# Performance work log

Measured on AMD Instinct MI355X. Metric: run time of the kernel, lower is better.

Reference implementation:

```python
import jax, jax.numpy as jnp
import numpy as np

NUM_HEADS = 16


def setup_inputs() -> dict:
    key = jax.random.key(0)
    k1, k2, k3 = jax.random.split(key, 3)
    B, S, D = 4, 2048, 1024
    hidden_states = jax.random.normal(k1, (B, S, D), dtype=jnp.float32)
    w_qkv = jax.random.normal(k2, (D, 3 * D), dtype=jnp.float32) * (1.0 / np.sqrt(D))
    w_out = jax.random.normal(k3, (D, D), dtype=jnp.float32) * (1.0 / np.sqrt(D))
    return {"hidden_states": hidden_states, "w_qkv": w_qkv, "w_out": w_out}


def reference(hidden_states, w_qkv, w_out):
    B, S, D = hidden_states.shape
    H = NUM_HEADS
    d = D // H
    # fused QKV projection: [B, S, 3D] -> [3, B, S, H, d]
    qkv = (hidden_states @ w_qkv).reshape(B, S, 3, H, d)
    q, k, v = jnp.moveaxis(qkv, 2, 0)  # each [B, S, H, d]
    scale = 1.0 / np.sqrt(d).astype(np.float32)
    scores = jnp.einsum("bqhd,bkhd->bhqk", q, k) * scale  # [B, H, S, S]
    attn = jax.nn.softmax(scores, axis=-1)
    ctx = jnp.einsum("bhqk,bkhd->bqhd", attn, v).reshape(B, S, D)
    return ctx @ w_out
```

## Files before the change

kernel.cpp:

```cpp
#include <hip/hip_runtime.h>
#include <hip/hip_bf16.h>
#include <math.h>

typedef __bf16 bf16;
typedef __bf16 bf16x4 __attribute__((ext_vector_type(4)));
typedef __bf16 bf16x8 __attribute__((ext_vector_type(8)));
typedef float  f32x4  __attribute__((ext_vector_type(4)));

#define B_  4
#define S_  2048
#define D_  1024
#define H_  16
#define DH  64
#define M_  (B_*S_)
#define BH_ (B_*H_)

#define QSCALE 0.18033688011112042f

__device__ __forceinline__ void glds16(const bf16* g, bf16* l) {
  __builtin_amdgcn_global_load_lds((const __attribute__((address_space(1))) void*)g,
                                   (__attribute__((address_space(3))) void*)l, 16, 0, 0);
}

__global__ __launch_bounds__(256) void prep(const float* __restrict__ hidden, bf16* __restrict__ hb,
                                            const float* __restrict__ wqkv, const float* __restrict__ wout,
                                            bf16* __restrict__ wqkvT, bf16* __restrict__ woutT) {
  int bx = blockIdx.x, tid = threadIdx.x;
  if (bx < 8192) {
    int i = (bx * 256 + tid) * 4;
    float4 v = *(const float4*)(hidden + i);
    bf16x4 o = { (bf16)v.x, (bf16)v.y, (bf16)v.z, (bf16)v.w };
    *(bf16x4*)(hb + i) = o;
    return;
  }
  __shared__ float tile[32][33];
  int t = bx - 8192;
  const float* in; bf16* out; int C, c0, r0;
  if (t < 96 * 32) { in = wqkv; out = wqkvT; C = 3072; c0 = (t % 96) * 32; r0 = (t / 96) * 32; }
  else { t -= 96 * 32;  in = wout; out = woutT; C = 1024; c0 = (t % 32) * 32; r0 = (t / 32) * 32; }
  int tx = tid & 31, ty = tid >> 5;
  #pragma unroll
  for (int i = ty; i < 32; i += 8) tile[i][tx] = in[(size_t)(r0 + i) * C + c0 + tx];
  __syncthreads();
  #pragma unroll
  for (int i = ty; i < 32; i += 8) out[(size_t)(c0 + i) * D_ + r0 + tx] = (bf16)tile[tx][i];
}

#define LDA2 32
#define SUB  (128 * LDA2)

__device__ __forceinline__ void gemm_core(const bf16* __restrict__ A, const bf16* __restrict__ Bt,
                                          int m0, int n0, bf16* As, bf16* Bs,
                                          int tid, f32x4 acc[4][4]) {
  int wave = tid >> 6, lane = tid & 63, quad = lane >> 4, l16 = lane & 15;
  int wm = (wave >> 1) * 64, wn = (wave & 1) * 64;
  int lr = lane >> 2, lc = (lane & 3) * 8;
  const bf16* gA = A  + (size_t)(m0 + wave * 32 + lr) * D_ + lc;
  const bf16* gB = Bt + (size_t)(n0 + wave * 32 + lr) * D_ + lc;
  bf16* lA = As + wave * 32 * LDA2;
  bf16* lB = Bs + wave * 32 * LDA2;
  for (int k0 = 0; k0 < D_; k0 += 64) {
    #pragma unroll
    for (int h = 0; h < 2; h++) {
      int kk = k0 + h * 32;
      glds16(gA + kk,           lA + h * SUB);
      glds16(gA + kk + 16 * D_, lA + h * SUB + 16 * LDA2);
      glds16(gB + kk,           lB + h * SUB);
      glds16(gB + kk + 16 * D_, lB + h * SUB + 16 * LDA2);
    }
    __syncthreads();
    #pragma unroll
    for (int h = 0; h < 2; h++) {
      bf16x8 af[4], bff[4];
      #pragma unroll
      for (int i = 0; i < 4; i++) af[i]  = *(const bf16x8*)(As + h * SUB + (wm + i * 16 + l16) * LDA2 + quad * 8);
      #pragma unroll
      for (int j = 0; j < 4; j++) bff[j] = *(const bf16x8*)(Bs + h * SUB + (wn + j * 16 + l16) * LDA2 + quad * 8);
      #pragma unroll
      for (int i = 0; i < 4; i++)
        #pragma unroll
        for (int j = 0; j < 4; j++)
          acc[i][j] = __builtin_amdgcn_mfma_f32_16x16x32_bf16(af[i], bff[j], acc[i][j], 0, 0, 0);
    }
    __syncthreads();
  }
}

__global__ __launch_bounds__(256) void gemm_qkv(const bf16* __restrict__ A, const bf16* __restrict__ Bt,
                                                bf16* __restrict__ Qb, bf16* __restrict__ Kb,
                                                bf16* __restrict__ Vtb) {
  __shared__ __attribute__((aligned(16))) bf16 As[2 * SUB];
  __shared__ __attribute__((aligned(16))) bf16 Bs[2 * SUB];
  int tid = threadIdx.x;
  int m0 = blockIdx.y * 128, n0 = blockIdx.x * 128;
  f32x4 acc[4][4] = {};
  gemm_core(A, Bt, m0, n0, As, Bs, tid, acc);
  int wave = tid >> 6, lane = tid & 63, quad = lane >> 4, l16 = lane & 15;
  int wm = (wave >> 1) * 64, wn = (wave & 1) * 64;
  int which = n0 >> 10;
  if (which == 2) {
    #pragma unroll
    for (int i = 0; i < 4; i++) {
      int mb = m0 + wm + i * 16 + quad * 4;
      int b = mb >> 11, s = mb & 2047;
      #pragma unroll
      for (int j = 0; j < 4; j++) {
        int n = n0 + wn + j * 16 + l16;
        int h = (n >> 6) & 15, dd = n & 63;
        bf16x4 v4 = { (bf16)acc[i][j][0], (bf16)acc[i][j][1], (bf16)acc[i][j][2], (bf16)acc[i][j][3] };
        *(bf16x4*)(Vtb + ((size_t)(b * H_ + h) * DH + dd) * S_ + s) = v4;
      }
    }
  } else {
    bf16* dst = (which == 0) ? Qb : Kb;
    float sc = (which == 0) ? QSCALE : 1.0f;
    #pragma unroll
    for (int i = 0; i < 4; i++) {
      #pragma unroll
      for (int j = 0; j < 4; j++) {
        int n = n0 + wn + j * 16 + l16;
        int h = (n >> 6) & 15, dd = n & 63;
        #pragma unroll
        for (int r = 0; r < 4; r++) {
          int m = m0 + wm + i * 16 + quad * 4 + r;
          int b = m >> 11, s = m & 2047;
          dst[(((size_t)(b * H_ + h)) * S_ + s) * DH + dd] = (bf16)(acc[i][j][r] * sc);
        }
      }
    }
  }
}

__global__ __launch_bounds__(256) void gemm_out(const bf16* __restrict__ A, const bf16* __restrict__ Bt,
                                                float* __restrict__ C) {
  __shared__ __attribute__((aligned(16))) bf16 As[2 * SUB];
  __shared__ __attribute__((aligned(16))) bf16 Bs[2 * SUB];
  int tid = threadIdx.x;
  int m0 = blockIdx.x * 128, n0 = blockIdx.y * 128;
  f32x4 acc[4][4] = {};
  gemm_core(A, Bt, m0, n0, As, Bs, tid, acc);
  int wave = tid >> 6, lane = tid & 63, quad = lane >> 4, l16 = lane & 15;
  int wm = (wave >> 1) * 64, wn = (wave & 1) * 64;
  #pragma unroll
  for (int i = 0; i < 4; i++)
    #pragma unroll
    for (int j = 0; j < 4; j++) {
      int n = n0 + wn + j * 16 + l16;
      #pragma unroll
      for (int r = 0; r < 4; r++) {
        int m = m0 + wm + i * 16 + quad * 4 + r;
        C[(size_t)m * D_ + n] = acc[i][j][r];
      }
    }
}

#define NT  (S_ / 64)

#define KVSW(row, col) (((row) * 64) + ((col) ^ (((row) & 7) << 3)))
#define PSW(row, col)  (((row) * 32) + ((col) ^ ((((row) >> 1) & 3) << 3)))

__global__ __launch_bounds__(256, 2) void attn(const bf16* __restrict__ Qb, const bf16* __restrict__ Kb,
                                               const bf16* __restrict__ Vtb, bf16* __restrict__ ctx) {
  __shared__ __attribute__((aligned(16))) bf16 Ks[2][64 * 64];
  __shared__ __attribute__((aligned(16))) bf16 Vs[2][64 * 64];
  __shared__ __attribute__((aligned(16))) bf16 Ps[4][64 * 32];
  int tid = threadIdx.x;
  int wave = tid >> 6, lane = tid & 63, quad = lane >> 4, l16 = lane & 15;
  int bh = blockIdx.x;
  int b = bh >> 4, h = bh & 15;
  int q0 = blockIdx.y * 256 + wave * 64;
  const bf16* Qp = Qb  + (size_t)bh * S_ * DH;
  const bf16* Kp = Kb  + (size_t)bh * S_ * DH;
  const bf16* Vp = Vtb + (size_t)bh * DH * S_;

  int srow = tid >> 3, scc = (tid & 7) << 3;
  int swz = KVSW(srow, scc);

  bf16x8 qf[4][2];
  #pragma unroll
  for (int nq = 0; nq < 4; nq++)
    #pragma unroll
    for (int ks = 0; ks < 2; ks++)
      qf[nq][ks] = *(const bf16x8*)(Qp + (size_t)(q0 + nq * 16 + l16) * DH + ks * 32 + quad * 8);

  bf16 one1 = (bf16)1.0f;
  bf16x8 onesf = { one1, one1, one1, one1, one1, one1, one1, one1 };

  f32x4 o[4][4] = {};
  f32x4 oden[4] = {};

  {
    bf16x8 k0a = *(const bf16x8*)(Kp + (size_t)srow * DH + scc);
    bf16x8 k0b = *(const bf16x8*)(Kp + (size_t)(32 + srow) * DH + scc);
    bf16x8 v0a = *(const bf16x8*)(Vp + (size_t)srow * S_ + scc);
    bf16x8 v0b = *(const bf16x8*)(Vp + (size_t)(32 + srow) * S_ + scc);
    *(bf16x8*)(Ks[0] + swz)             = k0a;
    *(bf16x8*)(Ks[0] + swz + 32 * 64)   = k0b;
    *(bf16x8*)(Vs[0] + swz)             = v0a;
    *(bf16x8*)(Vs[0] + swz + 32 * 64)   = v0b;
  }

  for (int kt = 0; kt < NT; kt++) {
    int cur = kt & 1;
    __syncthreads();

    bf16x8 ka, kb2, va, vb;
    if (kt + 1 < NT) {
      const bf16* Kn = Kp + (size_t)(kt + 1) * 64 * DH;
      const bf16* Vn = Vp + (size_t)(kt + 1) * 64;
      ka  = *(const bf16x8*)(Kn + (size_t)srow * DH + scc);
      kb2 = *(const bf16x8*)(Kn + (size_t)(32 + srow) * DH + scc);
      va  = *(const bf16x8*)(Vn + (size_t)srow * S_ + scc);
      vb  = *(const bf16x8*)(Vn + (size_t)(32 + srow) * S_ + scc);
    }

    bf16x8 vf[4][2];
    #pragma unroll
    for (int td = 0; td < 4; td++)
      #pragma unroll
      for (int ks = 0; ks < 2; ks++)
        vf[td][ks] = *(const bf16x8*)(Vs[cur] + KVSW(td * 16 + l16, ks * 32 + quad * 8));

    #pragma unroll
    for (int hh = 0; hh < 2; hh++) {
      #pragma unroll
      for (int kq2 = 0; kq2 < 2; kq2++) {
        int kq = hh * 2 + kq2;
        bf16x8 kfr[2];
        #pragma unroll
        for (int ks = 0; ks < 2; ks++)
          kfr[ks] = *(const bf16x8*)(Ks[cur] + KVSW(kq * 16 + l16, ks * 32 + quad * 8));
        #pragma unroll
        for (int nq = 0; nq < 4; nq++) {
          f32x4 st = {};
          __builtin_amdgcn_s_setprio(1);
          st = __builtin_amdgcn_mfma_f32_16x16x32_bf16(kfr[0], qf[nq][0], st, 0, 0, 0);
          st = __builtin_amdgcn_mfma_f32_16x16x32_bf16(kfr[1], qf[nq][1], st, 0, 0, 0);
          __builtin_amdgcn_s_setprio(0);
          bf16x4 pk;
          #pragma unroll
          for (int r = 0; r < 4; r++) pk[r] = (bf16)__builtin_amdgcn_exp2f(st[r]);
          *(bf16x4*)(&Ps[wave][PSW(nq * 16 + l16, kq2 * 16 + quad * 4)]) = pk;
        }
      }
      #pragma unroll
      for (int nq = 0; nq < 4; nq++) {
        bf16x8 pf = *(const bf16x8*)(&Ps[wave][PSW(nq * 16 + l16, quad * 8)]);
        __builtin_amdgcn_s_setprio(1);
        oden[nq] = __builtin_amdgcn_mfma_f32_16x16x32_bf16(pf, onesf, oden[nq], 0, 0, 0);
        #pragma unroll
        for (int td = 0; td < 4; td++)
          o[nq][td] = __builtin_amdgcn_mfma_f32_16x16x32_bf16(pf, vf[td][hh], o[nq][td], 0, 0, 0);
        __builtin_amdgcn_s_setprio(0);
      }
    }

    if (kt + 1 < NT) {
      int nxt = cur ^ 1;
      *(bf16x8*)(Ks[nxt] + swz)           = ka;
      *(bf16x8*)(Ks[nxt] + swz + 32 * 64) = kb2;
      *(bf16x8*)(Vs[nxt] + swz)           = va;
      *(bf16x8*)(Vs[nxt] + swz + 32 * 64) = vb;
    }
  }

  #pragma unroll
  for (int nq = 0; nq < 4; nq++) {
    #pragma unroll
    for (int r = 0; r < 4; r++) {
      float inv = 1.0f / oden[nq][r];
      int q = q0 + nq * 16 + quad * 4 + r;
      #pragma unroll
      for (int td = 0; td < 4; td++) {
        int dd = td * 16 + l16;
        ctx[((size_t)(b * S_) + q) * D_ + h * DH + dd] = (bf16)(o[nq][td][r] * inv);
      }
    }
  }
}

extern "C" void kernel_launch(void* const* d_in, const int* in_sizes, int n_in,
                              void* d_out, int out_size, void* d_ws, size_t ws_size,
                              hipStream_t stream) {
  (void)in_sizes; (void)n_in; (void)out_size; (void)ws_size;
  const float* hidden = (const float*)d_in[0];
  const float* w_qkv  = (const float*)d_in[1];
  const float* w_out  = (const float*)d_in[2];
  float* out = (float*)d_out;

  char* ws = (char*)d_ws;
  size_t off = 0;
  bf16* hb    = (bf16*)(ws + off); off += (size_t)M_ * D_ * 2;
  bf16* wqkvT = (bf16*)(ws + off); off += (size_t)3 * D_ * D_ * 2;
  bf16* woutT = (bf16*)(ws + off); off += (size_t)D_ * D_ * 2;
  bf16* Qb    = (bf16*)(ws + off); off += (size_t)M_ * D_ * 2;
  bf16* Kb    = (bf16*)(ws + off); off += (size_t)M_ * D_ * 2;
  bf16* Vtb   = (bf16*)(ws + off); off += (size_t)M_ * D_ * 2;
  bf16* ctxb  = hb;

  prep<<<8192 + 96 * 32 + 32 * 32, 256, 0, stream>>>(hidden, hb, w_qkv, w_out, wqkvT, woutT);
  gemm_qkv<<<dim3(3 * D_ / 128, M_ / 128), 256, 0, stream>>>(hb, wqkvT, Qb, Kb, Vtb);
  attn<<<dim3(BH_, S_ / 256), 256, 0, stream>>>(Qb, Kb, Vtb, ctxb);
  gemm_out<<<dim3(M_ / 128, D_ / 128), 256, 0, stream>>>(ctxb, woutT, out);
}
```

Baseline: 258.4 us.

## Fuse hidden fp32->bf16 cast into QKV GEMM, remap blocks, vectorize epilogues

The separate pass that casts hidden states to bf16 is removed; the QKV GEMM now loads fp32 A tiles directly, converts them in registers and writes them to LDS. Block indices are remapped so that neighbouring M tiles land on the same XCD for better L2 reuse. For Q/K and the output GEMM, the MFMA operands are swapped so the epilogues can write vectorized bf16x4 or f32x4 stores instead of scalar ones. The s_setprio hints are dropped from the attention loop. The fused A path loses the async global-to-LDS copy and reads twice the bytes per A tile inside the GEMM.

```diff
diff --git a/kernel.cpp b/kernel.cpp
--- a/kernel.cpp
+++ b/kernel.cpp
@@ -22,19 +22,10 @@
                                    (__attribute__((address_space(3))) void*)l, 16, 0, 0);
 }
 
-__global__ __launch_bounds__(256) void prep(const float* __restrict__ hidden, bf16* __restrict__ hb,
-                                            const float* __restrict__ wqkv, const float* __restrict__ wout,
+__global__ __launch_bounds__(256) void prep(const float* __restrict__ wqkv, const float* __restrict__ wout,
                                             bf16* __restrict__ wqkvT, bf16* __restrict__ woutT) {
-  int bx = blockIdx.x, tid = threadIdx.x;
-  if (bx < 8192) {
-    int i = (bx * 256 + tid) * 4;
-    float4 v = *(const float4*)(hidden + i);
-    bf16x4 o = { (bf16)v.x, (bf16)v.y, (bf16)v.z, (bf16)v.w };
-    *(bf16x4*)(hb + i) = o;
-    return;
-  }
   __shared__ float tile[32][33];
-  int t = bx - 8192;
+  int t = blockIdx.x, tid = threadIdx.x;
   const float* in; bf16* out; int C, c0, r0;
   if (t < 96 * 32) { in = wqkv; out = wqkvT; C = 3072; c0 = (t % 96) * 32; r0 = (t / 96) * 32; }
   else { t -= 96 * 32;  in = wout; out = woutT; C = 1024; c0 = (t % 32) * 32; r0 = (t / 32) * 32; }
@@ -49,9 +40,10 @@
 #define LDA2 32
 #define SUB  (128 * LDA2)
 
-__device__ __forceinline__ void gemm_core(const bf16* __restrict__ A, const bf16* __restrict__ Bt,
-                                          int m0, int n0, bf16* As, bf16* Bs,
-                                          int tid, f32x4 acc[4][4]) {
+template<bool SW>
+__device__ __forceinline__ void core128(const bf16* __restrict__ A, const bf16* __restrict__ Bt,
+                                        int m0, int n0, bf16* As, bf16* Bs,
+                                        int tid, f32x4 acc[4][4]) {
   int wave = tid >> 6, lane = tid & 63, quad = lane >> 4, l16 = lane & 15;
   int wm = (wave >> 1) * 64, wn = (wave & 1) * 64;
   int lr = lane >> 2, lc = (lane & 3) * 8;
@@ -79,26 +71,86 @@
       #pragma unroll
       for (int i = 0; i < 4; i++)
         #pragma unroll
-        for (int j = 0; j < 4; j++)
-          acc[i][j] = __builtin_amdgcn_mfma_f32_16x16x32_bf16(af[i], bff[j], acc[i][j], 0, 0, 0);
-    }
-    __syncthreads();
-  }
-}
-
-__global__ __launch_bounds__(256) void gemm_qkv(const bf16* __restrict__ A, const bf16* __restrict__ Bt,
+        for (int j = 0; j < 4; j++) {
+          if constexpr (SW)
+            acc[j][i] = __builtin_amdgcn_mfma_f32_16x16x32_bf16(bff[j], af[i], acc[j][i], 0, 0, 0);
+          else
+            acc[i][j] = __builtin_amdgcn_mfma_f32_16x16x32_bf16(af[i], bff[j], acc[i][j], 0, 0, 0);
+        }
+    }
+    __syncthreads();
+  }
+}
+
+template<bool SW>
+__device__ __forceinline__ void coreA32(const float* __restrict__ Af, const bf16* __restrict__ Bt,
+                                        int m0, int n0, bf16* As, bf16* Bs,
+                                        int tid, f32x4 acc[4][4]) {
+  int wave = tid >> 6, lane = tid & 63, quad = lane >> 4, l16 = lane & 15;
+  int wm = (wave >> 1) * 64, wn = (wave & 1) * 64;
+  int lr = lane >> 2, lc = (lane & 3) * 8;
+  const float* gA = Af + (size_t)(m0 + wave * 32 + lr) * D_ + lc;
+  const bf16*  gB = Bt + (size_t)(n0 + wave * 32 + lr) * D_ + lc;
+  bf16* lB = Bs + wave * 32 * LDA2;
+  bf16* wA = As + wave * 32 * LDA2 + lane * 8;
+  for (int k0 = 0; k0 < D_; k0 += 64) {
+    #pragma unroll
+    for (int h = 0; h < 2; h++) {
+      int kk = k0 + h * 32;
+      glds16(gB + kk,           lB + h * SUB);
+      glds16(gB + kk + 16 * D_, lB + h * SUB + 16 * LDA2);
+    }
+    #pragma unroll
+    for (int h = 0; h < 2; h++) {
+      int kk = k0 + h * 32;
+      #pragma unroll
+      for (int c = 0; c < 2; c++) {
+        const float* src = gA + kk + (size_t)(c * 16) * D_;
+        float4 v0 = *(const float4*)(src);
+        float4 v1 = *(const float4*)(src + 4);
+        bf16x8 w = { (bf16)v0.x, (bf16)v0.y, (bf16)v0.z, (bf16)v0.w,
+                     (bf16)v1.x, (bf16)v1.y, (bf16)v1.z, (bf16)v1.w };
+        *(bf16x8*)(wA + h * SUB + c * 16 * LDA2) = w;
+      }
+    }
+    __syncthreads();
+    #pragma unroll
+    for (int h = 0; h < 2; h++) {
+      bf16x8 af[4], bff[4];
+      #pragma unroll
+      for (int i = 0; i < 4; i++) af[i]  = *(const bf16x8*)(As + h * SUB + (wm + i * 16 + l16) * LDA2 + quad * 8);
+      #pragma unroll
+      for (int j = 0; j < 4; j++) bff[j] = *(const bf16x8*)(Bs + h * SUB + (wn + j * 16 + l16) * LDA2 + quad * 8);
+      #pragma unroll
+      for (int i = 0; i < 4; i++)
+        #pragma unroll
+        for (int j = 0; j < 4; j++) {
+          if constexpr (SW)
+            acc[j][i] = __builtin_amdgcn_mfma_f32_16x16x32_bf16(bff[j], af[i], acc[j][i], 0, 0, 0);
+          else
+            acc[i][j] = __builtin_amdgcn_mfma_f32_16x16x32_bf16(af[i], bff[j], acc[i][j], 0, 0, 0);
+        }
+    }
+    __syncthreads();
+  }
+}
+
+__global__ __launch_bounds__(256) void gemm_qkv(const float* __restrict__ hidden, const bf16* __restrict__ Bt,
                                                 bf16* __restrict__ Qb, bf16* __restrict__ Kb,
                                                 bf16* __restrict__ Vtb) {
   __shared__ __attribute__((aligned(16))) bf16 As[2 * SUB];
   __shared__ __attribute__((aligned(16))) bf16 Bs[2 * SUB];
   int tid = threadIdx.x;
-  int m0 = blockIdx.y * 128, n0 = blockIdx.x * 128;
-  f32x4 acc[4][4] = {};
-  gemm_core(A, Bt, m0, n0, As, Bs, tid, acc);
+  int lin = blockIdx.y * 24 + blockIdx.x;
+  int xcd = lin & 7, idx = lin >> 3;
+  int m0 = ((xcd << 3) + (idx / 24)) * 128;
+  int n0 = (idx % 24) * 128;
   int wave = tid >> 6, lane = tid & 63, quad = lane >> 4, l16 = lane & 15;
   int wm = (wave >> 1) * 64, wn = (wave & 1) * 64;
   int which = n0 >> 10;
+  f32x4 acc[4][4] = {};
   if (which == 2) {
+    coreA32<false>(hidden, Bt, m0, n0, As, Bs, tid, acc);
     #pragma unroll
     for (int i = 0; i < 4; i++) {
       int mb = m0 + wm + i * 16 + quad * 4;
@@ -112,20 +164,20 @@
       }
     }
   } else {
+    coreA32<true>(hidden, Bt, m0, n0, As, Bs, tid, acc);
     bf16* dst = (which == 0) ? Qb : Kb;
     float sc = (which == 0) ? QSCALE : 1.0f;
     #pragma unroll
     for (int i = 0; i < 4; i++) {
+      int m = m0 + wm + i * 16 + l16;
+      int b = m >> 11, s = m & 2047;
       #pragma unroll
       for (int j = 0; j < 4; j++) {
-        int n = n0 + wn + j * 16 + l16;
+        int n = n0 + wn + j * 16 + quad * 4;
         int h = (n >> 6) & 15, dd = n & 63;
-        #pragma unroll
-        for (int r = 0; r < 4; r++) {
-          int m = m0 + wm + i * 16 + quad * 4 + r;
-          int b = m >> 11, s = m & 2047;
-          dst[(((size_t)(b * H_ + h)) * S_ + s) * DH + dd] = (bf16)(acc[i][j][r] * sc);
-        }
+        bf16x4 v4 = { (bf16)(acc[j][i][0] * sc), (bf16)(acc[j][i][1] * sc),
+                      (bf16)(acc[j][i][2] * sc), (bf16)(acc[j][i][3] * sc) };
+        *(bf16x4*)(dst + (((size_t)(b * H_ + h)) * S_ + s) * DH + dd) = v4;
       }
     }
   }
@@ -138,20 +190,18 @@
   int tid = threadIdx.x;
   int m0 = blockIdx.x * 128, n0 = blockIdx.y * 128;
   f32x4 acc[4][4] = {};
-  gemm_core(A, Bt, m0, n0, As, Bs, tid, acc);
+  core128<true>(A, Bt, m0, n0, As, Bs, tid, acc);
   int wave = tid >> 6, lane = tid & 63, quad = lane >> 4, l16 = lane & 15;
   int wm = (wave >> 1) * 64, wn = (wave & 1) * 64;
   #pragma unroll
-  for (int i = 0; i < 4; i++)
+  for (int i = 0; i < 4; i++) {
+    int m = m0 + wm + i * 16 + l16;
     #pragma unroll
     for (int j = 0; j < 4; j++) {
-      int n = n0 + wn + j * 16 + l16;
-      #pragma unroll
-      for (int r = 0; r < 4; r++) {
-        int m = m0 + wm + i * 16 + quad * 4 + r;
-        C[(size_t)m * D_ + n] = acc[i][j][r];
-      }
-    }
+      int n = n0 + wn + j * 16 + quad * 4;
+      *(f32x4*)(&C[(size_t)m * D_ + n]) = acc[j][i];
+    }
+  }
 }
 
 #define NT  (S_ / 64)
@@ -233,10 +283,8 @@
         #pragma unroll
         for (int nq = 0; nq < 4; nq++) {
           f32x4 st = {};
-          __builtin_amdgcn_s_setprio(1);
           st = __builtin_amdgcn_mfma_f32_16x16x32_bf16(kfr[0], qf[nq][0], st, 0, 0, 0);
           st = __builtin_amdgcn_mfma_f32_16x16x32_bf16(kfr[1], qf[nq][1], st, 0, 0, 0);
-          __builtin_amdgcn_s_setprio(0);
           bf16x4 pk;
           #pragma unroll
           for (int r = 0; r < 4; r++) pk[r] = (bf16)__builtin_amdgcn_exp2f(st[r]);
@@ -246,12 +294,10 @@
       #pragma unroll
       for (int nq = 0; nq < 4; nq++) {
         bf16x8 pf = *(const bf16x8*)(&Ps[wave][PSW(nq * 16 + l16, quad * 8)]);
-        __builtin_amdgcn_s_setprio(1);
         oden[nq] = __builtin_amdgcn_mfma_f32_16x16x32_bf16(pf, onesf, oden[nq], 0, 0, 0);
         #pragma unroll
         for (int td = 0; td < 4; td++)
           o[nq][td] = __builtin_amdgcn_mfma_f32_16x16x32_bf16(pf, vf[td][hh], o[nq][td], 0, 0, 0);
-        __builtin_amdgcn_s_setprio(0);
       }
     }
 
@@ -290,16 +336,15 @@
 
   char* ws = (char*)d_ws;
   size_t off = 0;
-  bf16* hb    = (bf16*)(ws + off); off += (size_t)M_ * D_ * 2;
+  bf16* ctxb  = (bf16*)(ws + off); off += (size_t)M_ * D_ * 2;
   bf16* wqkvT = (bf16*)(ws + off); off += (size_t)3 * D_ * D_ * 2;
   bf16* woutT = (bf16*)(ws + off); off += (size_t)D_ * D_ * 2;
   bf16* Qb    = (bf16*)(ws + off); off += (size_t)M_ * D_ * 2;
   bf16* Kb    = (bf16*)(ws + off); off += (size_t)M_ * D_ * 2;
   bf16* Vtb   = (bf16*)(ws + off); off += (size_t)M_ * D_ * 2;
-  bf16* ctxb  = hb;
-
-  prep<<<8192 + 96 * 32 + 32 * 32, 256, 0, stream>>>(hidden, hb, w_qkv, w_out, wqkvT, woutT);
-  gemm_qkv<<<dim3(3 * D_ / 128, M_ / 128), 256, 0, stream>>>(hb, wqkvT, Qb, Kb, Vtb);
+
+  prep<<<96 * 32 + 32 * 32, 256, 0, stream>>>(w_qkv, w_out, wqkvT, woutT);
+  gemm_qkv<<<dim3(24, 64), 256, 0, stream>>>(hidden, wqkvT, Qb, Kb, Vtb);
   attn<<<dim3(BH_, S_ / 256), 256, 0, stream>>>(Qb, Kb, Vtb, ctxb);
   gemm_out<<<dim3(M_ / 128, D_ / 128), 256, 0, stream>>>(ctxb, woutT, out);
 }
```

Result: slower. 268.4 us (+3.9%).
